# Performance work log

Hardware: AMD Instinct MI355X
Metric: run time of the kernel (lower is better)

## Reference

```python
import jax, jax.numpy as jnp
import numpy as np

M, B, S = 8, 64, 1024
I = K = V = 256
H = 8
F = 1024


def setup_inputs() -> dict:
    key0 = jax.random.key(0)
    ks = iter(jax.random.split(key0, 64))
    nrm = lambda shp, s=1.0: jax.random.normal(next(ks), shp, dtype=jnp.float32) * s
    w = 0.05
    inp = {
        's0': nrm((M, B, I)), 'q0': nrm((M, B, K)), 'k0': nrm((M, B, K)), 'v0': nrm((M, B, V)),
        'key': nrm((S, B, K)), 'value': nrm((S, B, V)),
        'attn_wq': nrm((M, K, K), w), 'attn_wk': nrm((M, K, K), w), 'attn_wv': nrm((M, K, K), w),
        'attn_bq': nrm((M, K), w), 'attn_bk': nrm((M, K), w), 'attn_bv': nrm((M, K), w),
        'attn_wo': nrm((M, K, K), w), 'attn_bo': nrm((M, K), w),
    }
    for p, out in (('q', K), ('k', K), ('v', V), ('s', I)):
        inp[p + '_w1'] = nrm((M, 2 * I, F), w)
        inp[p + '_b1'] = nrm((M, F), w)
        inp[p + '_w2'] = nrm((M, F, out), w)
        inp[p + '_b2'] = nrm((M, out), w)
    inp['g_w1'] = nrm((4, M, 2 * I, F), w)
    inp['g_b1'] = nrm((4, M, F), w)
    inp['g_w2'] = nrm((4, M, F, 1), w)
    inp['g_b2'] = nrm((4, M, 1), w)
    return inp


def _forward(s0, q0, k0, v0, key, value,
             attn_wq, attn_wk, attn_wv, attn_bq, attn_bk, attn_bv, attn_wo, attn_bo,
             q_w1, q_b1, q_w2, q_b2, k_w1, k_b1, k_w2, k_b2,
             v_w1, v_b1, v_w2, v_b2, s_w1, s_b1, s_w2, s_b2,
             g_w1, g_b1, g_w2, g_b2):
    m, b, kd = q0.shape
    s = key.shape[0]
    hd = kd // H
    # per-module projections (single-query decode-style attention)
    q = jnp.einsum('mbk,mkd->mbd', q0, attn_wq) + attn_bq[:, None, :]          # (M,B,K)
    kk = jnp.einsum('sbk,mkd->msbd', key, attn_wk) + attn_bk[:, None, None, :]  # (M,S,B,K)
    vv = jnp.einsum('sbk,mkd->msbd', value, attn_wv) + attn_bv[:, None, None, :]
    qh = q.reshape(m, b, H, hd)
    kh = kk.reshape(m, s, b, H, hd)
    vh = vv.reshape(m, s, b, H, hd)
    scores = jnp.einsum('mbhd,msbhd->mbhs', qh, kh) / jnp.sqrt(jnp.float32(hd))
    aw = jax.nn.softmax(scores, axis=-1)                                        # (M,B,H,S)
    ctx = jnp.einsum('mbhs,msbhd->mbhd', aw, vh).reshape(m, b, kd)
    attn_out = jnp.einsum('mbk,mko->mbo', ctx, attn_wo) + attn_bo[:, None, :]   # (M,B,K)
    attn_weights = aw.mean(axis=2)                                              # (M,B,S)

    # _make_mlp puts ReLU FIRST: Seq(ReLU, Lin, ReLU, Lin, last_act)
    fc_in = jax.nn.relu(jnp.concatenate([attn_out, s0], axis=-1))               # (M,B,2I)

    def head(w1, b1, w2, b2):
        h = jax.nn.relu(jnp.einsum('mbi,mif->mbf', fc_in, w1) + b1[:, None, :])
        return jnp.einsum('mbf,mfo->mbo', h, w2) + b2[:, None, :]

    # non-gate heads: last activation ReLU, then .tanh() in forward
    oq = jnp.tanh(jax.nn.relu(head(q_w1, q_b1, q_w2, q_b2)))
    ok = jnp.tanh(jax.nn.relu(head(k_w1, k_b1, k_w2, k_b2)))
    ov = jnp.tanh(jax.nn.relu(head(v_w1, v_b1, v_w2, v_b2)))
    os_ = jnp.tanh(jax.nn.relu(head(s_w1, s_b1, s_w2, s_b2)))

    # gate heads stacked on leading g axis (query,key,value,state)
    gh = jax.nn.relu(jnp.einsum('mbi,gmif->gmbf', fc_in, g_w1) + g_b1[:, :, None, :])
    gates = jax.nn.sigmoid(jnp.einsum('gmbf,gmfo->gmbo', gh, g_w2) + g_b2[:, :, None, :])
    qg, kg, vg, sg = gates[0], gates[1], gates[2], gates[3]

    gq = qg * oq + (1.0 - qg) * q0
    gk = kg * ok + (1.0 - kg) * k0
    gv = vg * ov + (1.0 - vg) * v0
    gs = sg * os_ + (1.0 - sg) * s0
    return attn_out, attn_weights, gs, gq, gk, gv


def reference(s0, q0, k0, v0, key, value,
              attn_wq, attn_wk, attn_wv, attn_bq, attn_bk, attn_bv, attn_wo, attn_bo,
              q_w1, q_b1, q_w2, q_b2, k_w1, k_b1, k_w2, k_b2,
              v_w1, v_b1, v_w2, v_b2, s_w1, s_b1, s_w2, s_b2,
              g_w1, g_b1, g_w2, g_b2):
    return _forward(s0, q0, k0, v0, key, value,
                    attn_wq, attn_wk, attn_wv, attn_bq, attn_bk, attn_bv, attn_wo, attn_bo,
                    q_w1, q_b1, q_w2, q_b2, k_w1, k_b1, k_w2, k_b2,
                    v_w1, v_b1, v_w2, v_b2, s_w1, s_b1, s_w2, s_b2,
                    g_w1, g_b1, g_w2, g_b2)
```

## Files before the change

kernel.cpp:

```cpp
#include <hip/hip_runtime.h>
#include <math.h>

#define Mm 8
#define Bb 64
#define Ss 1024
#define Kk 256
#define Hh 8
#define HD 32
#define Ff 1024

#define WS_Q      0u
#define WS_U      131072u
#define WS_QDB    1179648u
#define WS_SC     1183744u
#define WS_WPART  5378048u
#define WS_FC     0u
#define WS_H1     5378048u
#define WS_GATES  262144u
#define WS_HPART  1183744u

__global__ __launch_bounds__(256) void k1_qproj(
    const float* __restrict__ q0, const float* __restrict__ wq,
    const float* __restrict__ bq, float* __restrict__ qout) {
  __shared__ float q0s[8 * 260];
  const int m = blockIdx.x, b0 = blockIdx.y * 8, t = threadIdx.x;
#pragma unroll
  for (int j = 0; j < 8; ++j)
    q0s[j * 260 + t] = q0[(m * Bb + b0 + j) * Kk + t];
  __syncthreads();
  float acc[8];
  const float bias = bq[m * Kk + t];
#pragma unroll
  for (int j = 0; j < 8; ++j) acc[j] = bias;
  const float* wcol = wq + m * Kk * Kk + t;
  for (int k4 = 0; k4 < Kk / 4; ++k4) {
    const float w0 = wcol[(k4 * 4 + 0) * Kk];
    const float w1 = wcol[(k4 * 4 + 1) * Kk];
    const float w2 = wcol[(k4 * 4 + 2) * Kk];
    const float w3 = wcol[(k4 * 4 + 3) * Kk];
#pragma unroll
    for (int j = 0; j < 8; ++j) {
      const float4 qv = *(const float4*)&q0s[j * 260 + k4 * 4];
      acc[j] += qv.x * w0 + qv.y * w1 + qv.z * w2 + qv.w * w3;
    }
  }
#pragma unroll
  for (int j = 0; j < 8; ++j)
    qout[(m * Bb + b0 + j) * Kk + t] = acc[j];
}

__global__ __launch_bounds__(256) void k2_uproj(
    const float* __restrict__ wk, const float* __restrict__ bk,
    const float* __restrict__ q, float* __restrict__ u,
    float* __restrict__ qdb) {
  __shared__ float qs[64 * 36];
  const int m = blockIdx.x, h = blockIdx.y, t = threadIdx.x;
#pragma unroll
  for (int p = 0; p < 8; ++p) {
    const int idx = p * 256 + t;
    const int d = idx & 31, b = idx >> 5;
    qs[b * 36 + d] = q[(m * Bb + b) * Kk + h * HD + d];
  }
  __syncthreads();
  float acc[64];
#pragma unroll
  for (int b = 0; b < 64; ++b) acc[b] = 0.f;
  const float* wrow = wk + (m * Kk + t) * Kk + h * HD;
#pragma unroll
  for (int d4 = 0; d4 < 8; ++d4) {
    const float4 w4 = *(const float4*)&wrow[d4 * 4];
#pragma unroll
    for (int b = 0; b < 64; ++b) {
      const float4 q4 = *(const float4*)&qs[b * 36 + d4 * 4];
      acc[b] += q4.x * w4.x + q4.y * w4.y + q4.z * w4.z + q4.w * w4.w;
    }
  }
  for (int b = 0; b < 64; ++b)
    u[((m * Bb + b) * Hh + h) * Kk + t] = acc[b];
  if (t < 64) {
    float s = 0.f;
#pragma unroll
    for (int d = 0; d < 32; ++d)
      s += qs[t * 36 + d] * bk[m * Kk + h * HD + d];
    qdb[(m * Bb + t) * Hh + h] = s;
  }
}

__global__ __launch_bounds__(256) void k3_scores(
    const float* __restrict__ key, const float* __restrict__ u,
    const float* __restrict__ qdb, float* __restrict__ sc) {
  __shared__ float us[32 * 260];
  __shared__ float kt[32 * 132];
  __shared__ float qd[32];
  const int b = blockIdx.x, mhh = blockIdx.y, s0 = blockIdx.z * 32,
            t = threadIdx.x;
  for (int p = 0; p < 32; ++p) {
    const int mh = mhh * 32 + p;
    us[p * 260 + t] = u[(((mh >> 3) * Bb + b) * Hh + (mh & 7)) * Kk + t];
  }
  if (t < 32) {
    const int mh = mhh * 32 + t;
    qd[t] = qdb[((mh >> 3) * Bb + b) * Hh + (mh & 7)];
  }
  float acc00 = 0.f, acc01 = 0.f, acc10 = 0.f, acc11 = 0.f;
  const int tmh = t & 15, ts = t >> 4;
  for (int kh = 0; kh < 2; ++kh) {
    __syncthreads();
#pragma unroll
    for (int p = 0; p < 16; ++p) {
      const int idx = p * 256 + t;
      const int k = idx & 127, sl = idx >> 7;
      kt[sl * 132 + k] = key[(s0 + sl) * (Bb * Kk) + b * Kk + kh * 128 + k];
    }
    __syncthreads();
#pragma unroll 8
    for (int k4 = 0; k4 < 32; ++k4) {
      const float4 u0 = *(const float4*)&us[tmh * 260 + kh * 128 + k4 * 4];
      const float4 u1 = *(const float4*)&us[(tmh + 16) * 260 + kh * 128 + k4 * 4];
      const float4 c0 = *(const float4*)&kt[(2 * ts) * 132 + k4 * 4];
      const float4 c1 = *(const float4*)&kt[(2 * ts + 1) * 132 + k4 * 4];
      acc00 += u0.x * c0.x + u0.y * c0.y + u0.z * c0.z + u0.w * c0.w;
      acc01 += u0.x * c1.x + u0.y * c1.y + u0.z * c1.z + u0.w * c1.w;
      acc10 += u1.x * c0.x + u1.y * c0.y + u1.z * c0.z + u1.w * c0.w;
      acc11 += u1.x * c1.x + u1.y * c1.y + u1.z * c1.z + u1.w * c1.w;
    }
  }
  const float scale = 0.17677669529663687f;
  const int mh0 = mhh * 32 + tmh, mh1 = mh0 + 16;
  const int r0 = ((mh0 >> 3) * Bb + b) * Hh + (mh0 & 7);
  const int r1 = ((mh1 >> 3) * Bb + b) * Hh + (mh1 & 7);
  const int s = s0 + 2 * ts;
  sc[r0 * Ss + s]     = (acc00 + qd[tmh]) * scale;
  sc[r0 * Ss + s + 1] = (acc01 + qd[tmh]) * scale;
  sc[r1 * Ss + s]     = (acc10 + qd[tmh + 16]) * scale;
  sc[r1 * Ss + s + 1] = (acc11 + qd[tmh + 16]) * scale;
}

__global__ __launch_bounds__(256) void k3b_softmax(float* __restrict__ sc,
                                                   float* __restrict__ out) {
  __shared__ float rows[8 * 1024];
  __shared__ float red[8];
  const int m = blockIdx.x, b = blockIdx.y, t = threadIdx.x;
  const int base = (m * Bb + b) * (Hh * Ss);
  for (int p = 0; p < 32; ++p)
    rows[p * 256 + t] = sc[base + p * 256 + t];
  __syncthreads();
  const int lane = t & 63, wid = t >> 6;
  for (int h = 0; h < 8; ++h) {
    float v0 = rows[h * 1024 + t], v1 = rows[h * 1024 + 256 + t],
          v2 = rows[h * 1024 + 512 + t], v3 = rows[h * 1024 + 768 + t];
    float mx = fmaxf(fmaxf(v0, v1), fmaxf(v2, v3));
    for (int off = 32; off > 0; off >>= 1)
      mx = fmaxf(mx, __shfl_down(mx, off, 64));
    if (lane == 0) red[wid] = mx;
    __syncthreads();
    mx = fmaxf(fmaxf(red[0], red[1]), fmaxf(red[2], red[3]));
    v0 = __expf(v0 - mx); v1 = __expf(v1 - mx);
    v2 = __expf(v2 - mx); v3 = __expf(v3 - mx);
    float sm = v0 + v1 + v2 + v3;
    for (int off = 32; off > 0; off >>= 1) sm += __shfl_down(sm, off, 64);
    if (lane == 0) red[4 + wid] = sm;
    __syncthreads();
    const float inv = 1.f / (red[4] + red[5] + red[6] + red[7]);
    v0 *= inv; v1 *= inv; v2 *= inv; v3 *= inv;
    rows[h * 1024 + t] = v0; rows[h * 1024 + 256 + t] = v1;
    rows[h * 1024 + 512 + t] = v2; rows[h * 1024 + 768 + t] = v3;
    sc[base + h * 1024 + t] = v0; sc[base + h * 1024 + 256 + t] = v1;
    sc[base + h * 1024 + 512 + t] = v2; sc[base + h * 1024 + 768 + t] = v3;
    __syncthreads();
  }
#pragma unroll
  for (int i = 0; i < 4; ++i) {
    const int s = i * 256 + t;
    float sum = 0.f;
#pragma unroll
    for (int h = 0; h < 8; ++h) sum += rows[h * 1024 + s];
    out[131072u + (m * Bb + b) * Ss + s] = sum * 0.125f;
  }
}

__global__ __launch_bounds__(256) void k4a_av(const float* __restrict__ value,
                                              const float* __restrict__ aw,
                                              float* __restrict__ wpart) {
  __shared__ float aws[32 * 36];
  __shared__ float vs[32 * 260];
  const int b = blockIdx.x, sc4 = blockIdx.y, mhh = blockIdx.z,
            t = threadIdx.x;
  const int tmh = t & 7, tk = t >> 3;
  float acc[4][8];
#pragma unroll
  for (int a = 0; a < 4; ++a)
#pragma unroll
    for (int j = 0; j < 8; ++j) acc[a][j] = 0.f;
  for (int st = 0; st < 8; ++st) {
    __syncthreads();
    const int s0 = sc4 * 256 + st * 32;
#pragma unroll
    for (int p = 0; p < 4; ++p) {
      const int idx = p * 256 + t;
      const int s = idx & 31, j = idx >> 5;
      const int mh = mhh * 32 + j;
      aws[j * 36 + s] =
          aw[(((mh >> 3) * Bb + b) * Hh + (mh & 7)) * Ss + s0 + s];
    }
#pragma unroll
    for (int p = 0; p < 32; ++p)
      vs[p * 260 + t] = value[(s0 + p) * (Bb * Kk) + b * Kk + t];
    __syncthreads();
#pragma unroll 2
    for (int s4 = 0; s4 < 8; ++s4) {
      float4 av[4];
#pragma unroll
      for (int a = 0; a < 4; ++a)
        av[a] = *(const float4*)&aws[(tmh + 8 * a) * 36 + s4 * 4];
#pragma unroll
      for (int ss = 0; ss < 4; ++ss) {
        const float4 v0 = *(const float4*)&vs[(s4 * 4 + ss) * 260 + tk * 4];
        const float4 v1 =
            *(const float4*)&vs[(s4 * 4 + ss) * 260 + 128 + tk * 4];
#pragma unroll
        for (int a = 0; a < 4; ++a) {
          const float aval = (ss == 0) ? av[a].x
                             : (ss == 1) ? av[a].y
                             : (ss == 2) ? av[a].z : av[a].w;
          acc[a][0] += aval * v0.x; acc[a][1] += aval * v0.y;
          acc[a][2] += aval * v0.z; acc[a][3] += aval * v0.w;
          acc[a][4] += aval * v1.x; acc[a][5] += aval * v1.y;
          acc[a][6] += aval * v1.z; acc[a][7] += aval * v1.w;
        }
      }
    }
  }
  float* wp = wpart + sc4 * 1048576u;
#pragma unroll
  for (int a = 0; a < 4; ++a) {
    const int mh = mhh * 32 + tmh + 8 * a;
    const int rb = (((mh >> 3) * Bb + b) * Hh + (mh & 7)) * Kk;
    float4 r0 = {acc[a][0], acc[a][1], acc[a][2], acc[a][3]};
    float4 r1 = {acc[a][4], acc[a][5], acc[a][6], acc[a][7]};
    *(float4*)&wp[rb + tk * 4] = r0;
    *(float4*)&wp[rb + 128 + tk * 4] = r1;
  }
}

__global__ __launch_bounds__(256) void k5_ctx(
    const float* __restrict__ wv, const float* __restrict__ bv,
    const float* __restrict__ wo, const float* __restrict__ bo,
    const float* __restrict__ s0in, const float* __restrict__ wpart,
    float* __restrict__ attn_out, float* __restrict__ fc) {
  __shared__ float wsh[2048];
  __shared__ float ctxs[256];
  const int m = blockIdx.x, b = blockIdx.y, t = threadIdx.x;
  const int base = (m * Bb + b) * (Hh * Kk);
#pragma unroll
  for (int p = 0; p < 8; ++p) {
    const int o = base + p * 256 + t;
    wsh[p * 256 + t] = wpart[o] + wpart[1048576u + o] + wpart[2097152u + o] +
                       wpart[3145728u + o];
  }
  __syncthreads();
  const int h = t >> 5;
  float acc = bv[m * Kk + t];
  const float* wvc = wv + m * Kk * Kk + t;
  for (int k4 = 0; k4 < 64; ++k4) {
    const float4 a4 = *(const float4*)&wsh[h * 256 + k4 * 4];
    acc += a4.x * wvc[(k4 * 4 + 0) * Kk] + a4.y * wvc[(k4 * 4 + 1) * Kk] +
           a4.z * wvc[(k4 * 4 + 2) * Kk] + a4.w * wvc[(k4 * 4 + 3) * Kk];
  }
  ctxs[t] = acc;
  __syncthreads();
  float acc2 = bo[m * Kk + t];
  const float* woc = wo + m * Kk * Kk + t;
  for (int k4 = 0; k4 < 64; ++k4) {
    const float4 c4 = *(const float4*)&ctxs[k4 * 4];
    acc2 += c4.x * woc[(k4 * 4 + 0) * Kk] + c4.y * woc[(k4 * 4 + 1) * Kk] +
            c4.z * woc[(k4 * 4 + 2) * Kk] + c4.w * woc[(k4 * 4 + 3) * Kk];
  }
  const int ob = (m * Bb + b) * Kk + t;
  attn_out[ob] = acc2;
  fc[(m * Bb + b) * 512 + t] = fmaxf(acc2, 0.f);
  fc[(m * Bb + b) * 512 + 256 + t] = fmaxf(s0in[ob], 0.f);
}

__global__ __launch_bounds__(256) void k6_mlp1(
    const float* __restrict__ fc, const float* __restrict__ w1q,
    const float* __restrict__ w1k, const float* __restrict__ w1v,
    const float* __restrict__ w1s, const float* __restrict__ w1g,
    const float* __restrict__ b1q, const float* __restrict__ b1k,
    const float* __restrict__ b1v, const float* __restrict__ b1s,
    const float* __restrict__ b1g, float* __restrict__ h1) {
  __shared__ float At[32 * 68];
  __shared__ float Wt[32 * 132];
  const int ft = blockIdx.x, m = blockIdx.y, head = blockIdx.z,
            t = threadIdx.x;
  const float* w1;
  const float* b1;
  if (head == 0)      { w1 = w1q; b1 = b1q; }
  else if (head == 1) { w1 = w1k; b1 = b1k; }
  else if (head == 2) { w1 = w1v; b1 = b1v; }
  else if (head == 3) { w1 = w1s; b1 = b1s; }
  else {
    w1 = w1g + (head - 4) * (Mm * 512 * Ff);
    b1 = b1g + (head - 4) * (Mm * Ff);
  }
  w1 += m * 512 * Ff;
  b1 += m * Ff;
  const int tf = t & 31, tb = t >> 5;
  float acc[8][4];
#pragma unroll
  for (int i = 0; i < 8; ++i)
#pragma unroll
    for (int j = 0; j < 4; ++j) acc[i][j] = 0.f;
  for (int it = 0; it < 16; ++it) {
    __syncthreads();
#pragma unroll
    for (int p = 0; p < 8; ++p) {
      const int idx = p * 256 + t;
      const int i = idx & 31, bb = idx >> 5;
      At[i * 68 + bb] = fc[(m * Bb + bb) * 512 + it * 32 + i];
    }
#pragma unroll
    for (int p = 0; p < 16; ++p) {
      const int idx = p * 256 + t;
      const int col = idx & 127, row = idx >> 7;
      Wt[row * 132 + col] = w1[(it * 32 + row) * Ff + ft * 128 + col];
    }
    __syncthreads();
#pragma unroll 4
    for (int kk = 0; kk < 32; ++kk) {
      const float4 a0 = *(const float4*)&At[kk * 68 + tb * 8];
      const float4 a1 = *(const float4*)&At[kk * 68 + tb * 8 + 4];
      const float4 w0 = *(const float4*)&Wt[kk * 132 + tf * 4];
      const float av[8] = {a0.x, a0.y, a0.z, a0.w, a1.x, a1.y, a1.z, a1.w};
#pragma unroll
      for (int i = 0; i < 8; ++i) {
        acc[i][0] += av[i] * w0.x; acc[i][1] += av[i] * w0.y;
        acc[i][2] += av[i] * w0.z; acc[i][3] += av[i] * w0.w;
      }
    }
  }
  const float4 bv0 = *(const float4*)&b1[ft * 128 + tf * 4];
  float* hb = h1 + (size_t)((head * Mm + m) * Bb) * Ff + ft * 128;
#pragma unroll
  for (int i = 0; i < 8; ++i) {
    const int bb = tb * 8 + i;
    float4 r0;
    r0.x = fmaxf(acc[i][0] + bv0.x, 0.f);
    r0.y = fmaxf(acc[i][1] + bv0.y, 0.f);
    r0.z = fmaxf(acc[i][2] + bv0.z, 0.f);
    r0.w = fmaxf(acc[i][3] + bv0.w, 0.f);
    *(float4*)&hb[bb * Ff + tf * 4] = r0;
  }
}

__global__ __launch_bounds__(64) void k6b_gates(
    const float* __restrict__ h1, const float* __restrict__ gw2,
    const float* __restrict__ gb2, float* __restrict__ gates) {
  const int gm = blockIdx.x, b = blockIdx.y, t = threadIdx.x;
  const int g = gm >> 3, m = gm & 7;
  const float* hrow = h1 + (size_t)(((4 + g) * Mm + m) * Bb + b) * Ff;
  const float* wrow = gw2 + (g * Mm + m) * Ff;
  float s = 0.f;
#pragma unroll
  for (int i = 0; i < 16; ++i) s += hrow[t + i * 64] * wrow[t + i * 64];
  for (int off = 32; off > 0; off >>= 1) s += __shfl_down(s, off, 64);
  if (t == 0)
    gates[(g * Mm + m) * Bb + b] =
        1.f / (1.f + __expf(-(s + gb2[g * Mm + m])));
}

__global__ __launch_bounds__(256) void k7a_mlp2(
    const float* __restrict__ h1, const float* __restrict__ w2q,
    const float* __restrict__ w2k, const float* __restrict__ w2v,
    const float* __restrict__ w2s, float* __restrict__ hpart) {
  __shared__ float Ht[32 * 68];
  __shared__ float Wt[32 * 68];
  const int fq = blockIdx.x >> 2, oc = blockIdx.x & 3;
  const int m = blockIdx.y, head = blockIdx.z, t = threadIdx.x;
  const float* w2 =
      (head == 0) ? w2q : (head == 1) ? w2k : (head == 2) ? w2v : w2s;
  w2 += (size_t)m * Ff * Kk;
  const float* hbase = h1 + (size_t)((head * Mm + m) * Bb) * Ff + fq * 256;
  const int to = t & 15, tb = t >> 4;
  float acc[4][4];
#pragma unroll
  for (int j = 0; j < 4; ++j)
#pragma unroll
    for (int i = 0; i < 4; ++i) acc[j][i] = 0.f;
  for (int it = 0; it < 8; ++it) {
    __syncthreads();
#pragma unroll
    for (int p = 0; p < 8; ++p) {
      const int idx = p * 256 + t;
      const int f = idx & 31, bb = idx >> 5;
      Ht[f * 68 + bb] = hbase[bb * Ff + it * 32 + f];
    }
#pragma unroll
    for (int p = 0; p < 8; ++p) {
      const int idx = p * 256 + t;
      const int o = idx & 63, f = idx >> 6;
      Wt[f * 68 + o] = w2[(fq * 256 + it * 32 + f) * Kk + oc * 64 + o];
    }
    __syncthreads();
#pragma unroll 8
    for (int kk = 0; kk < 32; ++kk) {
      const float4 a4 = *(const float4*)&Ht[kk * 68 + tb * 4];
      const float4 w4 = *(const float4*)&Wt[kk * 68 + to * 4];
      acc[0][0] += a4.x * w4.x; acc[0][1] += a4.x * w4.y;
      acc[0][2] += a4.x * w4.z; acc[0][3] += a4.x * w4.w;
      acc[1][0] += a4.y * w4.x; acc[1][1] += a4.y * w4.y;
      acc[1][2] += a4.y * w4.z; acc[1][3] += a4.y * w4.w;
      acc[2][0] += a4.z * w4.x; acc[2][1] += a4.z * w4.y;
      acc[2][2] += a4.z * w4.z; acc[2][3] += a4.z * w4.w;
      acc[3][0] += a4.w * w4.x; acc[3][1] += a4.w * w4.y;
      acc[3][2] += a4.w * w4.z; acc[3][3] += a4.w * w4.w;
    }
  }
  float* hp =
      hpart + fq * 524288u + (size_t)((head * Mm + m) * Bb) * Kk + oc * 64;
#pragma unroll
  for (int j = 0; j < 4; ++j) {
    const int bb = tb * 4 + j;
    float4 r = {acc[j][0], acc[j][1], acc[j][2], acc[j][3]};
    *(float4*)&hp[bb * Kk + to * 4] = r;
  }
}

__global__ __launch_bounds__(256) void k7b_final(
    const float* __restrict__ hpart, const float* __restrict__ gates,
    const float* __restrict__ b2q, const float* __restrict__ b2k,
    const float* __restrict__ b2v, const float* __restrict__ b2s,
    const float* __restrict__ q0, const float* __restrict__ k0,
    const float* __restrict__ v0, const float* __restrict__ s0,
    float* __restrict__ out) {
  const int idx = blockIdx.x * 256 + threadIdx.x;
  const int o = idx & 255;
  const int b = (idx >> 8) & 63;
  const int m = (idx >> 14) & 7;
  const int head = idx >> 17;
  const float* b2 = (head == 0) ? b2q : (head == 1) ? b2k
                    : (head == 2) ? b2v : b2s;
  const float* x0 = (head == 0) ? q0 : (head == 1) ? k0
                    : (head == 2) ? v0 : s0;
  const unsigned ooff = (head == 0) ? 786432u
                        : (head == 1) ? 917504u
                        : (head == 2) ? 1048576u : 655360u;
  float v = hpart[idx] + hpart[524288u + idx] + hpart[1048576u + idx] +
            hpart[1572864u + idx] + b2[m * Kk + o];
  v = tanhf(fmaxf(v, 0.f));
  const float g = gates[(head * Mm + m) * Bb + b];
  const float x = x0[(m * Bb + b) * Kk + o];
  out[ooff + (m * Bb + b) * Kk + o] = g * v + (1.f - g) * x;
}

extern "C" void kernel_launch(void* const* d_in, const int* in_sizes, int n_in,
                              void* d_out, int out_size, void* d_ws,
                              size_t ws_size, hipStream_t stream) {
  (void)in_sizes; (void)n_in; (void)out_size; (void)ws_size;
  const float* s0  = (const float*)d_in[0];
  const float* q0  = (const float*)d_in[1];
  const float* k0  = (const float*)d_in[2];
  const float* v0  = (const float*)d_in[3];
  const float* key = (const float*)d_in[4];
  const float* val = (const float*)d_in[5];
  const float* wq  = (const float*)d_in[6];
  const float* wk  = (const float*)d_in[7];
  const float* wv  = (const float*)d_in[8];
  const float* bqa = (const float*)d_in[9];
  const float* bka = (const float*)d_in[10];
  const float* bva = (const float*)d_in[11];
  const float* wo  = (const float*)d_in[12];
  const float* bo  = (const float*)d_in[13];
  const float* qw1 = (const float*)d_in[14];
  const float* qb1 = (const float*)d_in[15];
  const float* qw2 = (const float*)d_in[16];
  const float* qb2 = (const float*)d_in[17];
  const float* kw1 = (const float*)d_in[18];
  const float* kb1 = (const float*)d_in[19];
  const float* kw2 = (const float*)d_in[20];
  const float* kb2 = (const float*)d_in[21];
  const float* vw1 = (const float*)d_in[22];
  const float* vb1 = (const float*)d_in[23];
  const float* vw2 = (const float*)d_in[24];
  const float* vb2 = (const float*)d_in[25];
  const float* sw1 = (const float*)d_in[26];
  const float* sb1 = (const float*)d_in[27];
  const float* sw2 = (const float*)d_in[28];
  const float* sb2 = (const float*)d_in[29];
  const float* gw1 = (const float*)d_in[30];
  const float* gb1 = (const float*)d_in[31];
  const float* gw2 = (const float*)d_in[32];
  const float* gb2 = (const float*)d_in[33];
  float* ws  = (float*)d_ws;
  float* out = (float*)d_out;

  k1_qproj<<<dim3(8, 8), 256, 0, stream>>>(q0, wq, bqa, ws + WS_Q);
  k2_uproj<<<dim3(8, 8), 256, 0, stream>>>(wk, bka, ws + WS_Q, ws + WS_U,
                                           ws + WS_QDB);
  k3_scores<<<dim3(64, 2, 32), 256, 0, stream>>>(key, ws + WS_U, ws + WS_QDB,
                                                 ws + WS_SC);
  k3b_softmax<<<dim3(8, 64), 256, 0, stream>>>(ws + WS_SC, out);
  k4a_av<<<dim3(64, 4, 2), 256, 0, stream>>>(val, ws + WS_SC, ws + WS_WPART);
  k5_ctx<<<dim3(8, 64), 256, 0, stream>>>(wv, bva, wo, bo, s0, ws + WS_WPART,
                                          out, ws + WS_FC);
  k6_mlp1<<<dim3(8, 8, 8), 256, 0, stream>>>(ws + WS_FC, qw1, kw1, vw1, sw1,
                                             gw1, qb1, kb1, vb1, sb1, gb1,
                                             ws + WS_H1);
  k6b_gates<<<dim3(32, 64), 64, 0, stream>>>(ws + WS_H1, gw2, gb2,
                                             ws + WS_GATES);
  k7a_mlp2<<<dim3(16, 8, 4), 256, 0, stream>>>(ws + WS_H1, qw2, kw2, vw2, sw2,
                                               ws + WS_HPART);
  k7b_final<<<dim3(2048), 256, 0, stream>>>(ws + WS_HPART, ws + WS_GATES, qb2,
                                            kb2, vb2, sb2, q0, k0, v0, s0,
                                            out);
}
```

Baseline: 524.5 us.

## Use fp16 MFMA matrix cores for score and first MLP GEMMs

Rewrites the attention score kernel and the first MLP layer kernel to use 16x16x32 fp16 MFMA instructions instead of scalar fp32 FMA loops. Tiles are restaged in shared memory, and operands are converted to fp16 on the fly, with the MLP weights packed as half pairs. The score kernel's grid is reshaped so each block covers all 64 head-modules over 128 sequence positions. The aim is to cut the FP32 ALU time of these GEMMs, at the cost of fp16 rounding of the inputs, which may affect accuracy.

```diff
diff --git a/kernel.cpp b/kernel.cpp
--- a/kernel.cpp
+++ b/kernel.cpp
@@ -8,6 +8,9 @@
 #define Hh 8
 #define HD 32
 #define Ff 1024
+
+typedef _Float16 f16x8 __attribute__((ext_vector_type(8)));
+typedef float f32x4 __attribute__((ext_vector_type(4)));
 
 #define WS_Q      0u
 #define WS_U      131072u
@@ -89,51 +92,68 @@
 __global__ __launch_bounds__(256) void k3_scores(
     const float* __restrict__ key, const float* __restrict__ u,
     const float* __restrict__ qdb, float* __restrict__ sc) {
-  __shared__ float us[32 * 260];
-  __shared__ float kt[32 * 132];
-  __shared__ float qd[32];
-  const int b = blockIdx.x, mhh = blockIdx.y, s0 = blockIdx.z * 32,
-            t = threadIdx.x;
-  for (int p = 0; p < 32; ++p) {
-    const int mh = mhh * 32 + p;
-    us[p * 260 + t] = u[(((mh >> 3) * Bb + b) * Hh + (mh & 7)) * Kk + t];
-  }
-  if (t < 32) {
-    const int mh = mhh * 32 + t;
-    qd[t] = qdb[((mh >> 3) * Bb + b) * Hh + (mh & 7)];
-  }
-  float acc00 = 0.f, acc01 = 0.f, acc10 = 0.f, acc11 = 0.f;
-  const int tmh = t & 15, ts = t >> 4;
-  for (int kh = 0; kh < 2; ++kh) {
-    __syncthreads();
-#pragma unroll
-    for (int p = 0; p < 16; ++p) {
-      const int idx = p * 256 + t;
-      const int k = idx & 127, sl = idx >> 7;
-      kt[sl * 132 + k] = key[(s0 + sl) * (Bb * Kk) + b * Kk + kh * 128 + k];
-    }
-    __syncthreads();
-#pragma unroll 8
-    for (int k4 = 0; k4 < 32; ++k4) {
-      const float4 u0 = *(const float4*)&us[tmh * 260 + kh * 128 + k4 * 4];
-      const float4 u1 = *(const float4*)&us[(tmh + 16) * 260 + kh * 128 + k4 * 4];
-      const float4 c0 = *(const float4*)&kt[(2 * ts) * 132 + k4 * 4];
-      const float4 c1 = *(const float4*)&kt[(2 * ts + 1) * 132 + k4 * 4];
-      acc00 += u0.x * c0.x + u0.y * c0.y + u0.z * c0.z + u0.w * c0.w;
-      acc01 += u0.x * c1.x + u0.y * c1.y + u0.z * c1.z + u0.w * c1.w;
-      acc10 += u1.x * c0.x + u1.y * c0.y + u1.z * c0.z + u1.w * c0.w;
-      acc11 += u1.x * c1.x + u1.y * c1.y + u1.z * c1.z + u1.w * c1.w;
+  __shared__ float Us[64 * 36];
+  __shared__ float Ks[128 * 36];
+  __shared__ float qd[64];
+  const int b = blockIdx.x, st0 = blockIdx.y * 128, t = threadIdx.x;
+  const int w = t >> 6, lane = t & 63, quad = lane >> 4, l15 = lane & 15;
+  if (t < 64) qd[t] = qdb[((t >> 3) * Bb + b) * Hh + (t & 7)];
+  f32x4 acc[8];
+#pragma unroll
+  for (int i = 0; i < 8; ++i) acc[i] = (f32x4){0.f, 0.f, 0.f, 0.f};
+  for (int kt = 0; kt < 8; ++kt) {
+    __syncthreads();
+#pragma unroll
+    for (int p = 0; p < 2; ++p) {
+      const int idx = p * 256 + t;
+      const int mh = idx >> 3, k4 = idx & 7;
+      const float4 v = *(const float4*)&u[(((mh >> 3) * Bb + b) * Hh +
+                                           (mh & 7)) * Kk + kt * 32 + k4 * 4];
+      *(float4*)&Us[mh * 36 + k4 * 4] = v;
+    }
+#pragma unroll
+    for (int p = 0; p < 4; ++p) {
+      const int idx = p * 256 + t;
+      const int s = idx >> 3, k4 = idx & 7;
+      const float4 v = *(const float4*)&key[(size_t)(st0 + s) * (Bb * Kk) +
+                                            b * Kk + kt * 32 + k4 * 4];
+      *(float4*)&Ks[s * 36 + k4 * 4] = v;
+    }
+    __syncthreads();
+    f16x8 af;
+    {
+      const float4 a0 = *(const float4*)&Us[(w * 16 + l15) * 36 + quad * 8];
+      const float4 a1 =
+          *(const float4*)&Us[(w * 16 + l15) * 36 + quad * 8 + 4];
+      af[0] = (_Float16)a0.x; af[1] = (_Float16)a0.y;
+      af[2] = (_Float16)a0.z; af[3] = (_Float16)a0.w;
+      af[4] = (_Float16)a1.x; af[5] = (_Float16)a1.y;
+      af[6] = (_Float16)a1.z; af[7] = (_Float16)a1.w;
+    }
+#pragma unroll
+    for (int sf = 0; sf < 8; ++sf) {
+      const float4 b0 = *(const float4*)&Ks[(sf * 16 + l15) * 36 + quad * 8];
+      const float4 b1 =
+          *(const float4*)&Ks[(sf * 16 + l15) * 36 + quad * 8 + 4];
+      f16x8 bf;
+      bf[0] = (_Float16)b0.x; bf[1] = (_Float16)b0.y;
+      bf[2] = (_Float16)b0.z; bf[3] = (_Float16)b0.w;
+      bf[4] = (_Float16)b1.x; bf[5] = (_Float16)b1.y;
+      bf[6] = (_Float16)b1.z; bf[7] = (_Float16)b1.w;
+      acc[sf] = __builtin_amdgcn_mfma_f32_16x16x32_f16(af, bf, acc[sf], 0, 0, 0);
     }
   }
   const float scale = 0.17677669529663687f;
-  const int mh0 = mhh * 32 + tmh, mh1 = mh0 + 16;
-  const int r0 = ((mh0 >> 3) * Bb + b) * Hh + (mh0 & 7);
-  const int r1 = ((mh1 >> 3) * Bb + b) * Hh + (mh1 & 7);
-  const int s = s0 + 2 * ts;
-  sc[r0 * Ss + s]     = (acc00 + qd[tmh]) * scale;
-  sc[r0 * Ss + s + 1] = (acc01 + qd[tmh]) * scale;
-  sc[r1 * Ss + s]     = (acc10 + qd[tmh + 16]) * scale;
-  sc[r1 * Ss + s + 1] = (acc11 + qd[tmh + 16]) * scale;
+#pragma unroll
+  for (int sf = 0; sf < 8; ++sf) {
+    const int s = st0 + sf * 16 + l15;
+#pragma unroll
+    for (int r = 0; r < 4; ++r) {
+      const int mh = w * 16 + quad * 4 + r;
+      sc[(size_t)(((mh >> 3) * Bb + b) * Hh + (mh & 7)) * Ss + s] =
+          (acc[sf][r] + qd[mh]) * scale;
+    }
+  }
 }
 
 __global__ __launch_bounds__(256) void k3b_softmax(float* __restrict__ sc,
@@ -289,8 +309,8 @@
     const float* __restrict__ b1q, const float* __restrict__ b1k,
     const float* __restrict__ b1v, const float* __restrict__ b1s,
     const float* __restrict__ b1g, float* __restrict__ h1) {
-  __shared__ float At[32 * 68];
-  __shared__ float Wt[32 * 132];
+  __shared__ float As[64 * 36];
+  __shared__ unsigned Wp[128 * 20];
   const int ft = blockIdx.x, m = blockIdx.y, head = blockIdx.z,
             t = threadIdx.x;
   const float* w1;
@@ -300,56 +320,63 @@
   else if (head == 2) { w1 = w1v; b1 = b1v; }
   else if (head == 3) { w1 = w1s; b1 = b1s; }
   else {
-    w1 = w1g + (head - 4) * (Mm * 512 * Ff);
+    w1 = w1g + (size_t)(head - 4) * (Mm * 512 * Ff);
     b1 = b1g + (head - 4) * (Mm * Ff);
   }
-  w1 += m * 512 * Ff;
+  w1 += (size_t)m * 512 * Ff;
   b1 += m * Ff;
-  const int tf = t & 31, tb = t >> 5;
-  float acc[8][4];
-#pragma unroll
-  for (int i = 0; i < 8; ++i)
-#pragma unroll
-    for (int j = 0; j < 4; ++j) acc[i][j] = 0.f;
+  const int w = t >> 6, lane = t & 63, quad = lane >> 4, l15 = lane & 15;
+  f32x4 acc[8];
+#pragma unroll
+  for (int i = 0; i < 8; ++i) acc[i] = (f32x4){0.f, 0.f, 0.f, 0.f};
   for (int it = 0; it < 16; ++it) {
     __syncthreads();
 #pragma unroll
+    for (int p = 0; p < 2; ++p) {
+      const int idx = p * 256 + t;
+      const int bb = idx >> 3, k4 = idx & 7;
+      const float4 v =
+          *(const float4*)&fc[(m * Bb + bb) * 512 + it * 32 + k4 * 4];
+      *(float4*)&As[bb * 36 + k4 * 4] = v;
+    }
+#pragma unroll
     for (int p = 0; p < 8; ++p) {
       const int idx = p * 256 + t;
-      const int i = idx & 31, bb = idx >> 5;
-      At[i * 68 + bb] = fc[(m * Bb + bb) * 512 + it * 32 + i];
-    }
-#pragma unroll
-    for (int p = 0; p < 16; ++p) {
-      const int idx = p * 256 + t;
-      const int col = idx & 127, row = idx >> 7;
-      Wt[row * 132 + col] = w1[(it * 32 + row) * Ff + ft * 128 + col];
-    }
-    __syncthreads();
-#pragma unroll 4
-    for (int kk = 0; kk < 32; ++kk) {
-      const float4 a0 = *(const float4*)&At[kk * 68 + tb * 8];
-      const float4 a1 = *(const float4*)&At[kk * 68 + tb * 8 + 4];
-      const float4 w0 = *(const float4*)&Wt[kk * 132 + tf * 4];
-      const float av[8] = {a0.x, a0.y, a0.z, a0.w, a1.x, a1.y, a1.z, a1.w};
-#pragma unroll
-      for (int i = 0; i < 8; ++i) {
-        acc[i][0] += av[i] * w0.x; acc[i][1] += av[i] * w0.y;
-        acc[i][2] += av[i] * w0.z; acc[i][3] += av[i] * w0.w;
-      }
-    }
-  }
-  const float4 bv0 = *(const float4*)&b1[ft * 128 + tf * 4];
-  float* hb = h1 + (size_t)((head * Mm + m) * Bb) * Ff + ft * 128;
-#pragma unroll
-  for (int i = 0; i < 8; ++i) {
-    const int bb = tb * 8 + i;
-    float4 r0;
-    r0.x = fmaxf(acc[i][0] + bv0.x, 0.f);
-    r0.y = fmaxf(acc[i][1] + bv0.y, 0.f);
-    r0.z = fmaxf(acc[i][2] + bv0.z, 0.f);
-    r0.w = fmaxf(acc[i][3] + bv0.w, 0.f);
-    *(float4*)&hb[bb * Ff + tf * 4] = r0;
+      const int f = idx & 127, kp = idx >> 7;
+      const float w0 = w1[(size_t)(it * 32 + 2 * kp) * Ff + ft * 128 + f];
+      const float w1v = w1[(size_t)(it * 32 + 2 * kp + 1) * Ff + ft * 128 + f];
+      union { unsigned u; _Float16 h[2]; } pk;
+      pk.h[0] = (_Float16)w0;
+      pk.h[1] = (_Float16)w1v;
+      Wp[f * 20 + kp] = pk.u;
+    }
+    __syncthreads();
+    f16x8 af;
+    {
+      const float4 a0 = *(const float4*)&As[(w * 16 + l15) * 36 + quad * 8];
+      const float4 a1 =
+          *(const float4*)&As[(w * 16 + l15) * 36 + quad * 8 + 4];
+      af[0] = (_Float16)a0.x; af[1] = (_Float16)a0.y;
+      af[2] = (_Float16)a0.z; af[3] = (_Float16)a0.w;
+      af[4] = (_Float16)a1.x; af[5] = (_Float16)a1.y;
+      af[6] = (_Float16)a1.z; af[7] = (_Float16)a1.w;
+    }
+#pragma unroll
+    for (int nf = 0; nf < 8; ++nf) {
+      const f16x8 bf = *(const f16x8*)&Wp[(nf * 16 + l15) * 20 + quad * 4];
+      acc[nf] = __builtin_amdgcn_mfma_f32_16x16x32_f16(af, bf, acc[nf], 0, 0, 0);
+    }
+  }
+  float* hb = h1 + (size_t)((head * Mm + m) * Bb) * Ff;
+#pragma unroll
+  for (int nf = 0; nf < 8; ++nf) {
+    const int f = ft * 128 + nf * 16 + l15;
+    const float bias = b1[f];
+#pragma unroll
+    for (int r = 0; r < 4; ++r) {
+      const int bb = w * 16 + quad * 4 + r;
+      hb[(size_t)bb * Ff + f] = fmaxf(acc[nf][r] + bias, 0.f);
+    }
   }
 }
 
@@ -497,8 +524,8 @@
   k1_qproj<<<dim3(8, 8), 256, 0, stream>>>(q0, wq, bqa, ws + WS_Q);
   k2_uproj<<<dim3(8, 8), 256, 0, stream>>>(wk, bka, ws + WS_Q, ws + WS_U,
                                            ws + WS_QDB);
-  k3_scores<<<dim3(64, 2, 32), 256, 0, stream>>>(key, ws + WS_U, ws + WS_QDB,
-                                                 ws + WS_SC);
+  k3_scores<<<dim3(64, 8), 256, 0, stream>>>(key, ws + WS_U, ws + WS_QDB,
+                                             ws + WS_SC);
   k3b_softmax<<<dim3(8, 64), 256, 0, stream>>>(ws + WS_SC, out);
   k4a_av<<<dim3(64, 4, 2), 256, 0, stream>>>(val, ws + WS_SC, ws + WS_WPART);
   k5_ctx<<<dim3(8, 64), 256, 0, stream>>>(wv, bva, wo, bo, s0, ws + WS_WPART,
```

After: 531.4 us. No clear change (+1.3%).
